# Kernel optimization log

Measured on AMD Instinct MI355X. Metric: run time of the kernel, lower is better.

## Reference

```python
import jax, jax.numpy as jnp
import numpy as np

IN_F, OUT_F, RANK = 4096, 4096, 16
ALPHA = 32.0
SCALING = ALPHA / RANK


def setup_inputs() -> dict:
    key = jax.random.key(0)
    kx, kw, ka, kb = jax.random.split(key, 4)
    x = jax.random.normal(kx, (4, 2048, IN_F), dtype=jnp.float32)
    # base linear weight [out, in] (kaiming-uniform-like scale)
    bound_w = 1.0 / np.sqrt(IN_F)
    W = jax.random.uniform(kw, (OUT_F, IN_F), minval=-bound_w, maxval=bound_w, dtype=jnp.float32)
    # lora_A [rank, in]: kaiming uniform; lora_B [out, rank]: nonzero for testing
    bound_a = np.sqrt(6.0 / IN_F) / np.sqrt(1.0 + 5.0)
    lora_A = jax.random.uniform(ka, (RANK, IN_F), minval=-bound_a, maxval=bound_a, dtype=jnp.float32)
    lora_B = jax.random.normal(kb, (OUT_F, RANK), dtype=jnp.float32) * 0.02
    return {"x": x, "W": W, "lora_A": lora_A, "lora_B": lora_B}


def reference(x, W, lora_A, lora_B):
    # base: x @ W^T  -> [b, s, out]
    base = jnp.einsum("bsi,oi->bso", x, W)
    # low-rank path: (x @ A^T) @ B^T * scaling (dropout p=0 -> identity)
    r = jnp.einsum("bsi,ri->bsr", x, lora_A)  # [b, s, rank]
    lora = jnp.einsum("bsr,or->bso", r, lora_B) * SCALING
    return base + lora
```

## Files before the change

### kernel.cpp

```cpp
#include <hip/hip_runtime.h>
#include <stdint.h>
#include <stddef.h>

#define IN_F    4096
#define OUT_F   4096
#define MTOK    8192
#define RANK    16
#define SCALING 2.0f

typedef __attribute__((ext_vector_type(8))) short          bf16x8;
typedef __attribute__((ext_vector_type(4))) float          f32x4;
typedef __attribute__((ext_vector_type(4))) float          fl4;
typedef __attribute__((ext_vector_type(4))) unsigned short u16x4;
typedef __attribute__((ext_vector_type(8))) unsigned short u16x8;

static __device__ __forceinline__ unsigned short f2bf(float f) {
  union { float f; uint32_t u; } v; v.f = f;
  return (unsigned short)((v.u + 0x7fffu + ((v.u >> 16) & 1u)) >> 16);
}

static __device__ __forceinline__ void gload16(const void* g, void* l) {
  __builtin_amdgcn_global_load_lds(
      (const __attribute__((address_space(1))) uint32_t*)g,
      (__attribute__((address_space(3))) uint32_t*)l,
      16, 0, 0);
}

#define SBAR() __builtin_amdgcn_sched_barrier(0)
#define BARRIER() do { SBAR(); __builtin_amdgcn_s_barrier(); SBAR(); } while (0)

#define MERGE_BLKS (OUT_F / 4)

__global__ void prep_kernel(const float* __restrict__ x,
                            const float* __restrict__ W,
                            const float* __restrict__ lA,
                            const float* __restrict__ lB,
                            unsigned short* __restrict__ Weff,
                            unsigned short* __restrict__ xb) {
  __shared__ float Bs[4][RANK];
  if (blockIdx.x < MERGE_BLKS) {
    const int o0 = blockIdx.x * 4;
    if (threadIdx.x < 4 * RANK)
      Bs[threadIdx.x >> 4][threadIdx.x & 15] =
          lB[o0 * RANK + threadIdx.x] * SCALING;
    __syncthreads();
#pragma unroll
    for (int it = 0; it < 4; ++it) {
      const int c = threadIdx.x * 4 + it * 1024;
      fl4 w0 = *(const fl4*)(W + (size_t)(o0 + 0) * IN_F + c);
      fl4 w1 = *(const fl4*)(W + (size_t)(o0 + 1) * IN_F + c);
      fl4 w2 = *(const fl4*)(W + (size_t)(o0 + 2) * IN_F + c);
      fl4 w3 = *(const fl4*)(W + (size_t)(o0 + 3) * IN_F + c);
#pragma unroll
      for (int r = 0; r < RANK; ++r) {
        const fl4 a = *(const fl4*)(lA + (size_t)r * IN_F + c);
        const float b0 = Bs[0][r], b1 = Bs[1][r], b2 = Bs[2][r], b3 = Bs[3][r];
#pragma unroll
        for (int e = 0; e < 4; ++e) {
          w0[e] += b0 * a[e]; w1[e] += b1 * a[e];
          w2[e] += b2 * a[e]; w3[e] += b3 * a[e];
        }
      }
      u16x4 p0, p1, p2, p3;
#pragma unroll
      for (int e = 0; e < 4; ++e) {
        p0[e] = f2bf(w0[e]); p1[e] = f2bf(w1[e]);
        p2[e] = f2bf(w2[e]); p3[e] = f2bf(w3[e]);
      }
      *(u16x4*)(Weff + (size_t)(o0 + 0) * IN_F + c) = p0;
      *(u16x4*)(Weff + (size_t)(o0 + 1) * IN_F + c) = p1;
      *(u16x4*)(Weff + (size_t)(o0 + 2) * IN_F + c) = p2;
      *(u16x4*)(Weff + (size_t)(o0 + 3) * IN_F + c) = p3;
    }
  } else {
    const size_t i = ((size_t)(blockIdx.x - MERGE_BLKS) * 256 + threadIdx.x) * 8;
    const fl4 a = *(const fl4*)(x + i);
    const fl4 b = *(const fl4*)(x + i + 4);
    u16x8 p;
    p[0] = f2bf(a[0]); p[1] = f2bf(a[1]); p[2] = f2bf(a[2]); p[3] = f2bf(a[3]);
    p[4] = f2bf(b[0]); p[5] = f2bf(b[1]); p[6] = f2bf(b[2]); p[7] = f2bf(b[3]);
    *(u16x8*)(xb + i) = p;
  }
}

__global__ __launch_bounds__(512, 2) void gemm8p_kernel(
    const unsigned short* __restrict__ X,
    const unsigned short* __restrict__ Wf,
    float* __restrict__ Out) {
  __shared__ char lds[131072];
  const int tid  = threadIdx.x;
  const int lane = tid & 63;
  const int wave = tid >> 6;
  const int wr = wave >> 2;
  const int wc = wave & 3;
  const int fr = lane & 15;
  const int fq = lane >> 4;

  const int bid = blockIdx.x;
  const int tm  = (bid & 7) * 4 + ((bid >> 3) & 3);
  const int tn  = bid >> 5;
  const int m0 = tm << 8;
  const int n0 = tn << 8;

  const unsigned short* Ag = X  + (size_t)m0 * IN_F;
  const unsigned short* Bg = Wf + (size_t)n0 * IN_F;

  const int rIW = lane >> 3;
  const int csw = ((lane & 7) ^ rIW) << 3;

  const int aBase = wr * 16384 + fr * 128;
  const int bBase = 65536 + (wc >> 1) * 16384 + (wc & 1) * 8192 + fr * 128;
  const int cA0 = (fq << 4) ^ ((fr & 7) << 4);
  const int cA1 = cA0 ^ 64;

#define STAGE_A(C, BUF, K) do {                                                \
    const int _rh = (C) * 64 + (wave & 3) * 16;                                \
    const int _r0 = (wave >> 2) * 128 + _rh + rIW;                             \
    char* _d = lds + (BUF) * 32768 + (wave >> 2) * 16384 + _rh * 128 +         \
               (lane << 4);                                                    \
    gload16(Ag + (size_t)_r0 * IN_F + (K) + csw, _d);                          \
    gload16(Ag + (size_t)(_r0 + 8) * IN_F + (K) + csw, _d + 1024);             \
  } while (0)

#define STAGE_B(C, BUF, K) do {                                                \
    const int _s  = wave >> 1;                                                 \
    const int _rh = (_s & 1) * 64 + (C) * 32 + (wave & 1) * 16;                \
    const int _r0 = (_s >> 1) * 128 + _rh + rIW;                               \
    char* _d = lds + 65536 + (BUF) * 32768 + (_s >> 1) * 16384 + _rh * 128 +   \
               (lane << 4);                                                    \
    gload16(Bg + (size_t)_r0 * IN_F + (K) + csw, _d);                          \
    gload16(Bg + (size_t)(_r0 + 8) * IN_F + (K) + csw, _d + 1024);             \
  } while (0)

#define LDA(BUF, M, KK) (*(const bf16x8*)(lds + (BUF) * 32768 + aBase + (M) * 2048 + (KK)))
#define LDB(BUF, N, KK) (*(const bf16x8*)(lds + (BUF) * 32768 + bBase + (N) * 2048 + (KK)))

#define MFMA_Q(MB, NB, BR)                                                     \
  _Pragma("unroll")                                                            \
  for (int mi = 0; mi < 4; ++mi)                                               \
    _Pragma("unroll")                                                          \
    for (int ni = 0; ni < 2; ++ni) {                                           \
      acc[(MB)+mi][(NB)+ni] = __builtin_amdgcn_mfma_f32_16x16x32_bf16(a[mi*2],   BR[ni*2],   acc[(MB)+mi][(NB)+ni], 0, 0, 0); \
      acc[(MB)+mi][(NB)+ni] = __builtin_amdgcn_mfma_f32_16x16x32_bf16(a[mi*2+1], BR[ni*2+1], acc[(MB)+mi][(NB)+ni], 0, 0, 0); \
    }

#define TILE(BU, NB, KN, PF)                                                   \
  do {                                                                         \
    if (PF) { STAGE_B(0, NB, KN);                                              \
              asm volatile("s_waitcnt vmcnt(4)" ::: "memory"); }               \
    else    { asm volatile("s_waitcnt vmcnt(2)" ::: "memory"); }               \
    BARRIER();                                                                 \
    _Pragma("unroll")                                                          \
    for (int mi = 0; mi < 4; ++mi) { a[mi*2] = LDA(BU, mi, cA0); a[mi*2+1] = LDA(BU, mi, cA1); } \
    _Pragma("unroll")                                                          \
    for (int ni = 0; ni < 2; ++ni) { b0[ni*2] = LDB(BU, ni, cA0); b0[ni*2+1] = LDB(BU, ni, cA1); } \
    __builtin_amdgcn_s_setprio(1);                                             \
    MFMA_Q(0, 0, b0)                                                           \
    __builtin_amdgcn_s_setprio(0);                                             \
    _Pragma("unroll")                                                          \
    for (int ni = 0; ni < 2; ++ni) { b1[ni*2] = LDB(BU, 2+ni, cA0); b1[ni*2+1] = LDB(BU, 2+ni, cA1); } \
    if (PF) STAGE_B(1, NB, KN);                                                \
    __builtin_amdgcn_s_setprio(1);                                             \
    MFMA_Q(0, 2, b1)                                                           \
    __builtin_amdgcn_s_setprio(0);                                             \
    if (PF) { asm volatile("s_waitcnt vmcnt(4)" ::: "memory"); }               \
    else    { asm volatile("s_waitcnt vmcnt(0)" ::: "memory"); }               \
    BARRIER();                                                                 \
    _Pragma("unroll")                                                          \
    for (int mi = 0; mi < 4; ++mi) { a[mi*2] = LDA(BU, 4+mi, cA0); a[mi*2+1] = LDA(BU, 4+mi, cA1); } \
    if (PF) STAGE_A(0, NB, KN);                                                \
    __builtin_amdgcn_s_setprio(1);                                             \
    MFMA_Q(4, 2, b1)                                                           \
    __builtin_amdgcn_s_setprio(0);                                             \
    if (PF) STAGE_A(1, NB, KN);                                                \
    __builtin_amdgcn_s_setprio(1);                                             \
    MFMA_Q(4, 0, b0)                                                           \
    __builtin_amdgcn_s_setprio(0);                                             \
    BARRIER();                                                                 \
  } while (0)

  f32x4 acc[8][4];
#pragma unroll
  for (int i = 0; i < 8; ++i)
#pragma unroll
    for (int j = 0; j < 4; ++j) acc[i][j] = (f32x4){0.f, 0.f, 0.f, 0.f};

  bf16x8 a[8], b0[4], b1[4];

  STAGE_B(0, 0, 0); STAGE_B(1, 0, 0); STAGE_A(0, 0, 0); STAGE_A(1, 0, 0);

  for (int tt = 0; tt < 32; ++tt) {
    const int k1 = (tt << 7) + 64;
    const int k2 = k1 + 64;
    TILE(0, 1, k1, true);
    TILE(1, 0, k2, (k2 < IN_F));
  }

#pragma unroll
  for (int mi = 0; mi < 8; ++mi) {
    const int row0 = m0 + wr * 128 + mi * 16 + fq * 4;
#pragma unroll
    for (int ni = 0; ni < 4; ++ni) {
      const int col = n0 + wc * 64 + ni * 16 + fr;
#pragma unroll
      for (int j = 0; j < 4; ++j)
        Out[(size_t)(row0 + j) * OUT_F + col] = acc[mi][ni][j];
    }
  }
#undef STAGE_A
#undef STAGE_B
#undef LDA
#undef LDB
#undef MFMA_Q
#undef TILE
}

__global__ __launch_bounds__(256) void gemm_f32x_kernel(
    const float* __restrict__ X,
    const unsigned short* __restrict__ Weff,
    float* __restrict__ Out) {
  __shared__ unsigned short As[128][32];
  __shared__ unsigned short Bs[128][32];

  const int tid  = threadIdx.x;
  const int lane = tid & 63;
  const int wave = tid >> 6;
  const int wr = wave >> 1, wc = wave & 1;
  const int fr = lane & 15, fq = lane >> 4;

  const int bid = blockIdx.x;
  const int m0 = (bid & 63) * 128;
  const int n0 = (bid >> 6) * 128;

  f32x4 acc[4][4];
#pragma unroll
  for (int i = 0; i < 4; ++i)
#pragma unroll
    for (int j = 0; j < 4; ++j) acc[i][j] = (f32x4){0.f, 0.f, 0.f, 0.f};

  const int srow = tid >> 2;
  const int sseg = tid & 3;

  for (int k0 = 0; k0 < IN_F; k0 += 32) {
    if (k0) __syncthreads();
    {
      const unsigned short* gB = Weff + (size_t)(n0 + srow) * IN_F + k0 + sseg * 8;
      gload16(gB, &Bs[srow][sseg * 8]);
      gload16(gB + (size_t)64 * IN_F, &Bs[64 + srow][sseg * 8]);
    }
#pragma unroll
    for (int it = 0; it < 4; ++it) {
      const int c   = tid + it * 256;
      const int row = c >> 3;
      const int c4  = (c & 7) * 4;
      const fl4 v = *(const fl4*)(X + (size_t)(m0 + row) * IN_F + k0 + c4);
      u16x4 p;
      p[0] = f2bf(v[0]); p[1] = f2bf(v[1]); p[2] = f2bf(v[2]); p[3] = f2bf(v[3]);
      *(u16x4*)&As[row][c4] = p;
    }
    __syncthreads();

    bf16x8 af[4], bfm[4];
#pragma unroll
    for (int m = 0; m < 4; ++m)
      af[m] = *(const bf16x8*)&As[wr * 64 + m * 16 + fr][fq * 8];
#pragma unroll
    for (int n = 0; n < 4; ++n)
      bfm[n] = *(const bf16x8*)&Bs[wc * 64 + n * 16 + fr][fq * 8];
#pragma unroll
    for (int m = 0; m < 4; ++m)
#pragma unroll
      for (int n = 0; n < 4; ++n)
        acc[m][n] = __builtin_amdgcn_mfma_f32_16x16x32_bf16(af[m], bfm[n], acc[m][n], 0, 0, 0);
  }

#pragma unroll
  for (int m = 0; m < 4; ++m) {
    const int row0 = m0 + wr * 64 + m * 16 + fq * 4;
#pragma unroll
    for (int n = 0; n < 4; ++n) {
      const int col = n0 + wc * 64 + n * 16 + fr;
#pragma unroll
      for (int j = 0; j < 4; ++j)
        Out[(size_t)(row0 + j) * OUT_F + col] = acc[m][n][j];
    }
  }
}

__global__ void lora_r_kernel(const float* __restrict__ x,
                              const float* __restrict__ lA,
                              float* __restrict__ r) {
  const int idx = blockIdx.x * 256 + threadIdx.x;
  const int m = idx / RANK, rr = idx % RANK;
  float acc = 0.f;
  for (int k = 0; k < IN_F; ++k)
    acc += x[(size_t)m * IN_F + k] * lA[(size_t)rr * IN_F + k];
  r[idx] = acc * SCALING;
}

__global__ void naive_out_kernel(const float* __restrict__ x,
                                 const float* __restrict__ W,
                                 const float* __restrict__ lB,
                                 const float* __restrict__ r,
                                 float* __restrict__ out) {
  const size_t idx = (size_t)blockIdx.x * 256 + threadIdx.x;
  const int m = (int)(idx / OUT_F), n = (int)(idx % OUT_F);
  float acc = 0.f;
  for (int k = 0; k < IN_F; ++k)
    acc += x[(size_t)m * IN_F + k] * W[(size_t)n * IN_F + k];
#pragma unroll
  for (int rr = 0; rr < RANK; ++rr)
    acc += r[(size_t)m * RANK + rr] * lB[(size_t)n * RANK + rr];
  out[idx] = acc;
}

extern "C" void kernel_launch(void* const* d_in, const int* in_sizes, int n_in,
                              void* d_out, int out_size, void* d_ws, size_t ws_size,
                              hipStream_t stream) {
  const float* x  = (const float*)d_in[0];
  const float* W  = (const float*)d_in[1];
  const float* lA = (const float*)d_in[2];
  const float* lB = (const float*)d_in[3];
  float* out = (float*)d_out;

  const size_t weff_bytes = (size_t)OUT_F * IN_F * 2;
  const size_t xb_bytes   = (size_t)MTOK * IN_F * 2;

  if (ws_size >= weff_bytes + xb_bytes) {
    unsigned short* Weff = (unsigned short*)d_ws;
    unsigned short* xb   = (unsigned short*)((char*)d_ws + weff_bytes);
    const int conv_blocks = (int)((MTOK * (size_t)IN_F) / (256 * 8));
    prep_kernel<<<MERGE_BLKS + conv_blocks, 256, 0, stream>>>(x, W, lA, lB, Weff, xb);
    gemm8p_kernel<<<(MTOK / 256) * (OUT_F / 256), 512, 0, stream>>>(xb, Weff, out);
  } else if (ws_size >= weff_bytes) {
    unsigned short* Weff = (unsigned short*)d_ws;
    prep_kernel<<<MERGE_BLKS, 256, 0, stream>>>(x, W, lA, lB, Weff, (unsigned short*)0);
    gemm_f32x_kernel<<<(MTOK / 128) * (OUT_F / 128), 256, 0, stream>>>(x, Weff, out);
  } else {
    float* r = (float*)d_ws;
    lora_r_kernel<<<(MTOK * RANK) / 256, 256, 0, stream>>>(x, lA, r);
    naive_out_kernel<<<(size_t)MTOK * OUT_F / 256, 256, 0, stream>>>(x, W, lB, r, out);
  }
}
```

Before: 299.7 us.

## Shrink GEMM tile to 256x128 with BK=32 for higher occupancy

Reworks the main bf16 GEMM from 256x256 tiles with BK=64 and 128KB LDS to 256x128 tiles with BK=32 and 48KB LDS, raising launch bounds to four blocks per CU. Staging becomes one combined A/B load per thread with a new swizzle, and each half-tile does a single load-then-MFMA phase with no interleaving. The aim is more resident waves to hide memory latency. In exchange, arithmetic intensity per tile drops, the grid doubles, and there are twice as many barriers per K step.

```diff
diff --git a/kernel.cpp b/kernel.cpp
--- a/kernel.cpp
+++ b/kernel.cpp
@@ -83,11 +83,11 @@
   }
 }
 
-__global__ __launch_bounds__(512, 2) void gemm8p_kernel(
+__global__ __launch_bounds__(512, 4) void gemm8p_kernel(
     const unsigned short* __restrict__ X,
     const unsigned short* __restrict__ Wf,
     float* __restrict__ Out) {
-  __shared__ char lds[131072];
+  __shared__ char lds[49152];
   const int tid  = threadIdx.x;
   const int lane = tid & 63;
   const int wave = tid >> 6;
@@ -100,98 +100,60 @@
   const int tm  = (bid & 7) * 4 + ((bid >> 3) & 3);
   const int tn  = bid >> 5;
   const int m0 = tm << 8;
-  const int n0 = tn << 8;
-
-  const unsigned short* Ag = X  + (size_t)m0 * IN_F;
-  const unsigned short* Bg = Wf + (size_t)n0 * IN_F;
-
-  const int rIW = lane >> 3;
-  const int csw = ((lane & 7) ^ rIW) << 3;
-
-  const int aBase = wr * 16384 + fr * 128;
-  const int bBase = 65536 + (wc >> 1) * 16384 + (wc & 1) * 8192 + fr * 128;
-  const int cA0 = (fq << 4) ^ ((fr & 7) << 4);
-  const int cA1 = cA0 ^ 64;
-
-#define STAGE_A(C, BUF, K) do {                                                \
-    const int _rh = (C) * 64 + (wave & 3) * 16;                                \
-    const int _r0 = (wave >> 2) * 128 + _rh + rIW;                             \
-    char* _d = lds + (BUF) * 32768 + (wave >> 2) * 16384 + _rh * 128 +         \
-               (lane << 4);                                                    \
-    gload16(Ag + (size_t)_r0 * IN_F + (K) + csw, _d);                          \
-    gload16(Ag + (size_t)(_r0 + 8) * IN_F + (K) + csw, _d + 1024);             \
+  const int n0 = tn << 7;
+
+  const int srow = tid >> 2;
+  const int sseg = lane & 3;
+  const int csw  = (sseg ^ ((lane >> 3) & 3)) * 8;
+  const unsigned short* AgT = X  + (size_t)(m0 + srow) * IN_F + csw;
+  const unsigned short* BgT = Wf + (size_t)(n0 + srow) * IN_F + csw;
+
+  const int rs   = (fq ^ ((fr >> 1) & 3)) << 4;
+  const int aOff = fr * 64 + rs;
+  const int bOff = 32768 + wc * 2048 + fr * 64 + rs;
+
+#define STAGE(BUF, K) do {                                                     \
+    char* _dA = lds + (BUF) * 16384 + tid * 16;                                \
+    gload16(AgT + (K), _dA);                                                   \
+    gload16(AgT + (size_t)128 * IN_F + (K), _dA + 8192);                       \
+    gload16(BgT + (K), lds + 32768 + (BUF) * 8192 + tid * 16);                 \
   } while (0)
 
-#define STAGE_B(C, BUF, K) do {                                                \
-    const int _s  = wave >> 1;                                                 \
-    const int _rh = (_s & 1) * 64 + (C) * 32 + (wave & 1) * 16;                \
-    const int _r0 = (_s >> 1) * 128 + _rh + rIW;                               \
-    char* _d = lds + 65536 + (BUF) * 32768 + (_s >> 1) * 16384 + _rh * 128 +   \
-               (lane << 4);                                                    \
-    gload16(Bg + (size_t)_r0 * IN_F + (K) + csw, _d);                          \
-    gload16(Bg + (size_t)(_r0 + 8) * IN_F + (K) + csw, _d + 1024);             \
-  } while (0)
-
-#define LDA(BUF, M, KK) (*(const bf16x8*)(lds + (BUF) * 32768 + aBase + (M) * 2048 + (KK)))
-#define LDB(BUF, N, KK) (*(const bf16x8*)(lds + (BUF) * 32768 + bBase + (N) * 2048 + (KK)))
-
-#define MFMA_Q(MB, NB, BR)                                                     \
-  _Pragma("unroll")                                                            \
-  for (int mi = 0; mi < 4; ++mi)                                               \
-    _Pragma("unroll")                                                          \
-    for (int ni = 0; ni < 2; ++ni) {                                           \
-      acc[(MB)+mi][(NB)+ni] = __builtin_amdgcn_mfma_f32_16x16x32_bf16(a[mi*2],   BR[ni*2],   acc[(MB)+mi][(NB)+ni], 0, 0, 0); \
-      acc[(MB)+mi][(NB)+ni] = __builtin_amdgcn_mfma_f32_16x16x32_bf16(a[mi*2+1], BR[ni*2+1], acc[(MB)+mi][(NB)+ni], 0, 0, 0); \
-    }
+#define LDA(BUF, MI) (*(const bf16x8*)(lds + (BUF) * 16384 + wr * 8192 + (MI) * 1024 + aOff))
+#define LDB(BUF, NI) (*(const bf16x8*)(lds + (BUF) * 8192 + (NI) * 1024 + bOff))
 
 #define TILE(BU, NB, KN, PF)                                                   \
   do {                                                                         \
-    if (PF) { STAGE_B(0, NB, KN);                                              \
-              asm volatile("s_waitcnt vmcnt(4)" ::: "memory"); }               \
-    else    { asm volatile("s_waitcnt vmcnt(2)" ::: "memory"); }               \
-    BARRIER();                                                                 \
-    _Pragma("unroll")                                                          \
-    for (int mi = 0; mi < 4; ++mi) { a[mi*2] = LDA(BU, mi, cA0); a[mi*2+1] = LDA(BU, mi, cA1); } \
-    _Pragma("unroll")                                                          \
-    for (int ni = 0; ni < 2; ++ni) { b0[ni*2] = LDB(BU, ni, cA0); b0[ni*2+1] = LDB(BU, ni, cA1); } \
-    __builtin_amdgcn_s_setprio(1);                                             \
-    MFMA_Q(0, 0, b0)                                                           \
-    __builtin_amdgcn_s_setprio(0);                                             \
-    _Pragma("unroll")                                                          \
-    for (int ni = 0; ni < 2; ++ni) { b1[ni*2] = LDB(BU, 2+ni, cA0); b1[ni*2+1] = LDB(BU, 2+ni, cA1); } \
-    if (PF) STAGE_B(1, NB, KN);                                                \
-    __builtin_amdgcn_s_setprio(1);                                             \
-    MFMA_Q(0, 2, b1)                                                           \
-    __builtin_amdgcn_s_setprio(0);                                             \
-    if (PF) { asm volatile("s_waitcnt vmcnt(4)" ::: "memory"); }               \
+    if (PF) { STAGE(NB, KN);                                                   \
+              asm volatile("s_waitcnt vmcnt(3)" ::: "memory"); }               \
     else    { asm volatile("s_waitcnt vmcnt(0)" ::: "memory"); }               \
     BARRIER();                                                                 \
     _Pragma("unroll")                                                          \
-    for (int mi = 0; mi < 4; ++mi) { a[mi*2] = LDA(BU, 4+mi, cA0); a[mi*2+1] = LDA(BU, 4+mi, cA1); } \
-    if (PF) STAGE_A(0, NB, KN);                                                \
+    for (int mi = 0; mi < 8; ++mi) a[mi] = LDA(BU, mi);                        \
+    b[0] = LDB(BU, 0); b[1] = LDB(BU, 1);                                      \
     __builtin_amdgcn_s_setprio(1);                                             \
-    MFMA_Q(4, 2, b1)                                                           \
-    __builtin_amdgcn_s_setprio(0);                                             \
-    if (PF) STAGE_A(1, NB, KN);                                                \
-    __builtin_amdgcn_s_setprio(1);                                             \
-    MFMA_Q(4, 0, b0)                                                           \
+    _Pragma("unroll")                                                          \
+    for (int mi = 0; mi < 8; ++mi)                                             \
+      _Pragma("unroll")                                                        \
+      for (int ni = 0; ni < 2; ++ni)                                           \
+        acc[mi][ni] = __builtin_amdgcn_mfma_f32_16x16x32_bf16(a[mi], b[ni], acc[mi][ni], 0, 0, 0); \
     __builtin_amdgcn_s_setprio(0);                                             \
     BARRIER();                                                                 \
   } while (0)
 
-  f32x4 acc[8][4];
+  f32x4 acc[8][2];
 #pragma unroll
   for (int i = 0; i < 8; ++i)
 #pragma unroll
-    for (int j = 0; j < 4; ++j) acc[i][j] = (f32x4){0.f, 0.f, 0.f, 0.f};
-
-  bf16x8 a[8], b0[4], b1[4];
-
-  STAGE_B(0, 0, 0); STAGE_B(1, 0, 0); STAGE_A(0, 0, 0); STAGE_A(1, 0, 0);
-
-  for (int tt = 0; tt < 32; ++tt) {
-    const int k1 = (tt << 7) + 64;
-    const int k2 = k1 + 64;
+    for (int j = 0; j < 2; ++j) acc[i][j] = (f32x4){0.f, 0.f, 0.f, 0.f};
+
+  bf16x8 a[8], b[2];
+
+  STAGE(0, 0);
+
+  for (int tt = 0; tt < 64; ++tt) {
+    const int k1 = (tt << 6) + 32;
+    const int k2 = k1 + 32;
     TILE(0, 1, k1, true);
     TILE(1, 0, k2, (k2 < IN_F));
   }
@@ -200,18 +162,16 @@
   for (int mi = 0; mi < 8; ++mi) {
     const int row0 = m0 + wr * 128 + mi * 16 + fq * 4;
 #pragma unroll
-    for (int ni = 0; ni < 4; ++ni) {
-      const int col = n0 + wc * 64 + ni * 16 + fr;
+    for (int ni = 0; ni < 2; ++ni) {
+      const int col = n0 + wc * 32 + ni * 16 + fr;
 #pragma unroll
       for (int j = 0; j < 4; ++j)
         Out[(size_t)(row0 + j) * OUT_F + col] = acc[mi][ni][j];
     }
   }
-#undef STAGE_A
-#undef STAGE_B
+#undef STAGE
 #undef LDA
 #undef LDB
-#undef MFMA_Q
 #undef TILE
 }
 
@@ -331,7 +291,7 @@
     unsigned short* xb   = (unsigned short*)((char*)d_ws + weff_bytes);
     const int conv_blocks = (int)((MTOK * (size_t)IN_F) / (256 * 8));
     prep_kernel<<<MERGE_BLKS + conv_blocks, 256, 0, stream>>>(x, W, lA, lB, Weff, xb);
-    gemm8p_kernel<<<(MTOK / 256) * (OUT_F / 256), 512, 0, stream>>>(xb, Weff, out);
+    gemm8p_kernel<<<(MTOK / 256) * (OUT_F / 128), 512, 0, stream>>>(xb, Weff, out);
   } else if (ws_size >= weff_bytes) {
     unsigned short* Weff = (unsigned short*)d_ws;
     prep_kernel<<<MERGE_BLKS, 256, 0, stream>>>(x, W, lA, lB, Weff, (unsigned short*)0);
```

New measurement: 343.4 us. 1.15x slower.
